# Optimization experiments

Hardware: AMD Instinct MI355X
Metric: run time of the kernel (lower is better)

Reference implementation:

```python
import jax, jax.numpy as jnp
import numpy as np

B = 32768   # batch
D = 1024    # input_dimension
H = 2048    # hidden width (layer_sizes = [2048, 2048])
LN_EPS = 1e-5


def _layer_norm(h, g, b):
    m = jnp.mean(h, axis=-1, keepdims=True)
    v = jnp.var(h, axis=-1, keepdims=True)
    return (h - m) * jax.lax.rsqrt(v + LN_EPS) * g + b


def setup_inputs() -> dict:
    key = jax.random.key(0)
    ks = jax.random.split(key, 5)
    s1 = 1.0 / np.sqrt(D)
    s2 = 1.0 / np.sqrt(H)
    return {
        "x": jax.random.normal(ks[0], (B, D), dtype=jnp.float32),
        "W1": jax.random.uniform(ks[1], (D, H), jnp.float32, -s1, s1),
        "b1": jax.random.uniform(ks[2], (H,), jnp.float32, -s1, s1),
        "g1": jnp.ones((H,), jnp.float32),
        "be1": jnp.zeros((H,), jnp.float32),
        "W2": jax.random.uniform(ks[3], (H, 9), jnp.float32, -s2, s2),
        "b2": jax.random.uniform(ks[4], (9,), jnp.float32, -s2, s2),
        "g2": jnp.ones((9,), jnp.float32),
        "be2": jnp.zeros((9,), jnp.float32),
    }


def reference(x, W1, b1, g1, be1, W2, b2, g2, be2):
    # MLP: Linear -> ReLU -> LayerNorm, twice (final width 9)
    h = _layer_norm(jax.nn.relu(x @ W1 + b1), g1, be1)      # [B, H]
    r = _layer_norm(jax.nn.relu(h @ W2 + b2), g2, be2)      # [B, 9]
    R = r.reshape(x.shape[0], 3, 3)                          # [B, 3, 3]
    # SVD projection onto SO(3): U @ diag(1,1,det(U Vh)) @ Vh
    U, _, Vh = jnp.linalg.svd(R, full_matrices=False)
    d = jnp.linalg.det(U @ Vh)                               # [B]
    scale = jnp.stack([jnp.ones_like(d), jnp.ones_like(d), d], axis=-1)  # [B,3]
    return (U * scale[:, None, :]) @ Vh                      # scale last col of U
```

## Files before the change

### kernel.cpp

```cpp
#include <hip/hip_runtime.h>

typedef unsigned short u16;
typedef _Float16 f16x8 __attribute__((ext_vector_type(8)));
typedef float f32x4 __attribute__((ext_vector_type(4)));

#define GLD16(gptr, lptr)                                                              \
  __builtin_amdgcn_global_load_lds((const __attribute__((address_space(1))) void*)(gptr), \
                                   (__attribute__((address_space(3))) void*)(lptr), 16, 0, 0)

#define MFMA_F16(a, b, c) __builtin_amdgcn_mfma_f32_16x16x32_f16((a), (b), (c), 0, 0, 0)

__global__ __launch_bounds__(256) void k_split_w1t(const float* __restrict__ w1,
                                                   u16* __restrict__ wh, u16* __restrict__ wl) {
  __shared__ float tile[32][33];
  int bn = blockIdx.x & 63;
  int bk = blockIdx.x >> 6;
  int tn = threadIdx.x & 31, tq = threadIdx.x >> 5;
#pragma unroll
  for (int r = 0; r < 4; ++r) {
    int k = bk * 32 + tq + r * 8;
    tile[tq + r * 8][tn] = w1[(size_t)k * 2048 + bn * 32 + tn];
  }
  __syncthreads();
#pragma unroll
  for (int r = 0; r < 4; ++r) {
    int n = bn * 32 + tq + r * 8;
    float v = tile[tn][tq + r * 8];
    _Float16 hi = (_Float16)v;
    _Float16 lo = (_Float16)(v - (float)hi);
    int qp = (tn >> 3) ^ ((n >> 1) & 3);
    int kp = bk * 32 + qp * 8 + (tn & 7);
    wh[(size_t)n * 1024 + kp] = __builtin_bit_cast(u16, hi);
    wl[(size_t)n * 1024 + kp] = __builtin_bit_cast(u16, lo);
  }
}

__global__ __launch_bounds__(256) void k_w2frag(const float* __restrict__ w2, const float* __restrict__ g1,
                                                u16* __restrict__ fh, u16* __restrict__ fl) {
  int t = blockIdx.x * 256 + threadIdx.x;
  int c = t >> 6, l = t & 63;
  int col = l & 15, lg = l >> 4;
  f16x8 H, L;
#pragma unroll
  for (int j = 0; j < 8; ++j) {
    int k = c * 32 + lg * 8 + j;
    float v = (col < 9) ? g1[k] * w2[k * 9 + col] : 0.f;
    _Float16 hi = (_Float16)v;
    H[j] = hi;
    L[j] = (_Float16)(v - (float)hi);
  }
  *(f16x8*)(fh + (size_t)t * 8) = H;
  *(f16x8*)(fl + (size_t)t * 8) = L;
}

__global__ void k_cgcb(const float* __restrict__ w2, const float* __restrict__ g1,
                       const float* __restrict__ be1, double* __restrict__ cgcb) {
  int l = threadIdx.x;
  double cg[9], cb[9];
#pragma unroll
  for (int j = 0; j < 9; ++j) { cg[j] = 0.0; cb[j] = 0.0; }
  for (int i = 0; i < 32; ++i) {
    int k = i * 64 + l;
    double g = (double)g1[k], b = (double)be1[k];
#pragma unroll
    for (int j = 0; j < 9; ++j) {
      double w = (double)w2[k * 9 + j];
      cg[j] += g * w;
      cb[j] += b * w;
    }
  }
  for (int off = 32; off; off >>= 1) {
#pragma unroll
    for (int j = 0; j < 9; ++j) {
      cg[j] += __shfl_xor(cg[j], off, 64);
      cb[j] += __shfl_xor(cb[j], off, 64);
    }
  }
  if (l == 0) {
    for (int j = 0; j < 16; ++j) {
      cgcb[j] = (j < 9) ? cg[j] : 0.0;
      cgcb[16 + j] = (j < 9) ? cb[j] : 0.0;
    }
  }
}

__global__ __launch_bounds__(512, 2) void k_gemm1(const float* __restrict__ x,
                                                  const u16* __restrict__ wh, const u16* __restrict__ wl,
                                                  const float* __restrict__ b1,
                                                  const u16* __restrict__ fh, const u16* __restrict__ fl,
                                                  float* __restrict__ pdot, float* __restrict__ pstat) {
  __shared__ __align__(16) u16 lds[2][32768];
  const int tid = threadIdx.x;
  const int swz = ((blockIdx.x & 7) << 7) | (blockIdx.x >> 3);
  const int m0 = (swz >> 3) << 8;
  const int n0 = (swz & 7) << 8;
  const int lane = tid & 63, w = tid >> 6;
  const int wr = (w >> 2) << 7;
  const int wc = (w & 3) << 6;
  const int lr = lane & 15, lg = lane >> 4;

  int a_off0[8], a_off1[8];
#pragma unroll
  for (int i = 0; i < 8; ++i) {
    int row = wr + i * 16 + lr;
    a_off0[i] = row * 32 + (((2 * lg) ^ (row & 7)) << 2);
    a_off1[i] = row * 32 + (((2 * lg + 1) ^ (row & 7)) << 2);
  }
  int b_off[4];
#pragma unroll
  for (int j = 0; j < 4; ++j) {
    int row = wc + j * 16 + lr;
    b_off[j] = row * 32 + ((lg ^ ((row >> 1) & 3)) << 3);
  }

  const size_t sA = (size_t)(m0 + (tid >> 3)) * 1024 + ((((tid & 7) ^ ((tid >> 3) & 7))) << 2);
  const size_t boff = (size_t)(n0 + (tid >> 2)) * 1024 + ((tid & 3) << 3);

#define STAGE_A(bf, kk)                                       \
  do {                                                        \
    GLD16(x + sA + (kk),          &lds[bf][tid * 8]);         \
    GLD16(x + sA + 65536 + (kk),  &lds[bf][4096 + tid * 8]);  \
    GLD16(x + sA + 131072 + (kk), &lds[bf][8192 + tid * 8]);  \
    GLD16(x + sA + 196608 + (kk), &lds[bf][12288 + tid * 8]); \
  } while (0)
#define STAGE_B(bf, rb, src, kk)                                       \
  do {                                                                 \
    GLD16((src) + boff + (kk),          &lds[bf][(rb) + tid * 8]);     \
    GLD16((src) + boff + 131072 + (kk), &lds[bf][(rb) + 4096 + tid * 8]); \
  } while (0)

  STAGE_A(0, 0);
  STAGE_B(0, 16384, wh, 0);
  STAGE_B(0, 24576, wl, 0);

  f32x4 acc[8][4] = {};
#pragma unroll 2
  for (int kt = 0; kt < 32; ++kt) {
    const int cur = kt & 1, nxt = cur ^ 1;
    const int nk = (kt < 31 ? kt + 1 : 31) * 32;
    STAGE_A(nxt, nk);
    asm volatile("s_waitcnt vmcnt(4)" ::: "memory");
    __builtin_amdgcn_s_barrier();
    asm volatile("" ::: "memory");
    const float* Ax = (const float*)&lds[cur][0];
    const u16* Bh = &lds[cur][16384];
    const u16* Bl = &lds[cur][24576];
    f16x8 bhf[4], blf[4], ahf[4], alf[4];

#define RD_B(j)                                         \
  do {                                                  \
    bhf[j] = *(const f16x8*)(Bh + b_off[j]);            \
    blf[j] = *(const f16x8*)(Bl + b_off[j]);            \
  } while (0)
#define RD_A(s, i)                                                    \
  do {                                                                \
    float4 fa = *(const float4*)(Ax + a_off0[i]);                     \
    float4 fb = *(const float4*)(Ax + a_off1[i]);                     \
    float ff[8] = {fa.x, fa.y, fa.z, fa.w, fb.x, fb.y, fb.z, fb.w};   \
    _Pragma("unroll")                                                 \
    for (int e = 0; e < 8; ++e) {                                     \
      _Float16 hi = (_Float16)ff[e];                                  \
      ahf[s][e] = hi;                                                 \
      alf[s][e] = (_Float16)(ff[e] - (float)hi);                      \
    }                                                                 \
  } while (0)
#define MM(s, i, j)                                     \
  do {                                                  \
    acc[i][j] = MFMA_F16(ahf[s], bhf[j], acc[i][j]);    \
    acc[i][j] = MFMA_F16(ahf[s], blf[j], acc[i][j]);    \
    acc[i][j] = MFMA_F16(alf[s], bhf[j], acc[i][j]);    \
  } while (0)
#define PRIO1 __builtin_amdgcn_s_setprio(1)
#define PRIO0 __builtin_amdgcn_s_setprio(0)

    RD_B(0); RD_A(0, 0);
    PRIO1; MM(0, 0, 0); PRIO0;
    RD_A(1, 1);
    PRIO1; MM(1, 1, 0); PRIO0;
    RD_B(1);
    STAGE_B(nxt, 16384, wh, nk);
    PRIO1; MM(0, 0, 1); MM(1, 1, 1); PRIO0;
    RD_A(2, 2);
    PRIO1; MM(2, 2, 0); MM(2, 2, 1); PRIO0;
    RD_A(3, 3);
    PRIO1; MM(3, 3, 0); MM(3, 3, 1); PRIO0;
    RD_B(2);
    STAGE_B(nxt, 24576, wl, nk);
    PRIO1; MM(0, 0, 2); MM(1, 1, 2); MM(2, 2, 2); MM(3, 3, 2); PRIO0;
    RD_B(3);
    PRIO1; MM(0, 0, 3); MM(1, 1, 3); MM(2, 2, 3); MM(3, 3, 3); PRIO0;
    RD_A(0, 4);
    PRIO1; MM(0, 4, 0); MM(0, 4, 1); MM(0, 4, 2); MM(0, 4, 3); PRIO0;
    RD_A(1, 5);
    PRIO1; MM(1, 5, 0); MM(1, 5, 1); MM(1, 5, 2); MM(1, 5, 3); PRIO0;
    RD_A(2, 6);
    PRIO1; MM(2, 6, 0); MM(2, 6, 1); MM(2, 6, 2); MM(2, 6, 3); PRIO0;
    RD_A(3, 7);
    PRIO1; MM(3, 7, 0); MM(3, 7, 1); MM(3, 7, 2); MM(3, 7, 3); PRIO0;
#undef RD_B
#undef RD_A
#undef MM
#undef PRIO1
#undef PRIO0
    asm volatile("" ::: "memory");
    __builtin_amdgcn_s_barrier();
  }
#undef STAGE_A
#undef STAGE_B

  asm volatile("s_waitcnt vmcnt(0)" ::: "memory");
  __syncthreads();
  float* vt = (float*)&lds[0][0];

#pragma unroll
  for (int j = 0; j < 4; ++j) {
    const float bias = b1[n0 + wc + j * 16 + lr];
#pragma unroll
    for (int i = 0; i < 8; ++i)
#pragma unroll
      for (int r = 0; r < 4; ++r) acc[i][j][r] = fmaxf(acc[i][j][r] + bias, 0.f);
  }

  f32x4 acc2[2] = {};
  float sstat[2] = {0.f, 0.f}, qstat[2] = {0.f, 0.f};
  const int myrow0 = w * 32;

#pragma unroll
  for (int half = 0; half < 2; ++half) {
    if (((w & 3) >> 1) == half) {
      const int colbase = wc & 127;
#pragma unroll
      for (int j = 0; j < 4; ++j) {
        const int lcol = colbase + j * 16 + lr;
        const int g = lcol >> 2, wsel = lcol & 3;
#pragma unroll
        for (int i = 0; i < 8; ++i)
#pragma unroll
          for (int r = 0; r < 4; ++r) {
            const int row = wr + i * 16 + lg * 4 + r;
            vt[row * 128 + ((g ^ (row & 7)) << 2) + wsel] = acc[i][j][r];
          }
      }
    }
    __syncthreads();
#pragma unroll
    for (int cl = 0; cl < 4; ++cl) {
      const int cglob = (n0 >> 5) + half * 4 + cl;
      const f16x8 bh = *(const f16x8*)(fh + (size_t)(cglob * 64 + lane) * 8);
      const f16x8 bl = *(const f16x8*)(fl + (size_t)(cglob * 64 + lane) * 8);
#pragma unroll
      for (int g2 = 0; g2 < 2; ++g2) {
        const int row = myrow0 + g2 * 16 + lr;
        const int g0 = cl * 8 + lg * 2;
        const float4 f0 = *(const float4*)&vt[row * 128 + ((g0 ^ (row & 7)) << 2)];
        const float4 f1 = *(const float4*)&vt[row * 128 + (((g0 + 1) ^ (row & 7)) << 2)];
        float f[8] = {f0.x, f0.y, f0.z, f0.w, f1.x, f1.y, f1.z, f1.w};
        f16x8 AH, AL;
#pragma unroll
        for (int e = 0; e < 8; ++e) {
          sstat[g2] += f[e];
          qstat[g2] = fmaf(f[e], f[e], qstat[g2]);
          _Float16 hi = (_Float16)f[e];
          AH[e] = hi;
          AL[e] = (_Float16)(f[e] - (float)hi);
        }
        acc2[g2] = MFMA_F16(AH, bh, acc2[g2]);
        acc2[g2] = MFMA_F16(AH, bl, acc2[g2]);
        acc2[g2] = MFMA_F16(AL, bh, acc2[g2]);
      }
    }
    __syncthreads();
  }

#pragma unroll
  for (int g2 = 0; g2 < 2; ++g2) {
    sstat[g2] += __shfl_xor(sstat[g2], 16, 64);
    sstat[g2] += __shfl_xor(sstat[g2], 32, 64);
    qstat[g2] += __shfl_xor(qstat[g2], 16, 64);
    qstat[g2] += __shfl_xor(qstat[g2], 32, 64);
  }
  const int ntile = n0 >> 8;
#pragma unroll
  for (int g2 = 0; g2 < 2; ++g2) {
    if (lg == 0) {
      const int row = m0 + myrow0 + g2 * 16 + lr;
      *(float2*)&pstat[((size_t)row * 8 + ntile) * 2] = make_float2(sstat[g2], qstat[g2]);
    }
    if (lr < 9) {
#pragma unroll
      for (int r = 0; r < 4; ++r) {
        const int row = m0 + myrow0 + g2 * 16 + lg * 4 + r;
        pdot[((size_t)row * 8 + ntile) * 12 + lr] = acc2[g2][r];
      }
    }
  }
}

static __device__ __forceinline__ void jrot(double S[3][3], double V[3][3], int p, int q, int r) {
  double apq = S[p][q];
  if (apq == 0.0) return;
  double tau = (S[q][q] - S[p][p]) / (2.0 * apq);
  double t = (tau >= 0.0 ? 1.0 : -1.0) / (fabs(tau) + sqrt(1.0 + tau * tau));
  double c = 1.0 / sqrt(1.0 + t * t);
  double s = t * c;
  double spp = S[p][p], sqq = S[q][q];
  double srp = S[r][p], srq = S[r][q];
  S[p][p] = spp - t * apq;
  S[q][q] = sqq + t * apq;
  S[p][q] = 0.0; S[q][p] = 0.0;
  S[r][p] = c * srp - s * srq; S[p][r] = S[r][p];
  S[r][q] = s * srp + c * srq; S[q][r] = S[r][q];
#pragma unroll
  for (int i = 0; i < 3; ++i) {
    double vip = V[i][p], viq = V[i][q];
    V[i][p] = c * vip - s * viq;
    V[i][q] = s * vip + c * viq;
  }
}

static __device__ void svd_so3(const double* Rf, float* Of) {
  double A[3][3], S[3][3];
  double V[3][3] = {{1, 0, 0}, {0, 1, 0}, {0, 0, 1}};
#pragma unroll
  for (int i = 0; i < 3; ++i)
#pragma unroll
    for (int j = 0; j < 3; ++j) A[i][j] = Rf[i * 3 + j];
#pragma unroll
  for (int p = 0; p < 3; ++p)
#pragma unroll
    for (int q = 0; q < 3; ++q) {
      double sa = 0.0;
#pragma unroll
      for (int i = 0; i < 3; ++i) sa += A[i][p] * A[i][q];
      S[p][q] = sa;
    }
  for (int it = 0; it < 6; ++it) {
    jrot(S, V, 0, 1, 2);
    jrot(S, V, 0, 2, 1);
    jrot(S, V, 1, 2, 0);
  }
  double l0 = S[0][0], l1 = S[1][1], l2 = S[2][2];
  double c0[3] = {V[0][0], V[1][0], V[2][0]};
  double c1[3] = {V[0][1], V[1][1], V[2][1]};
  double c2[3] = {V[0][2], V[1][2], V[2][2]};
  double tl, tv;
#define SWP(la, lb, ca, cb)                                         \
  if (la < lb) {                                                    \
    tl = la; la = lb; lb = tl;                                      \
    tv = ca[0]; ca[0] = cb[0]; cb[0] = tv;                          \
    tv = ca[1]; ca[1] = cb[1]; cb[1] = tv;                          \
    tv = ca[2]; ca[2] = cb[2]; cb[2] = tv;                          \
  }
  SWP(l0, l1, c0, c1)
  SWP(l0, l2, c0, c2)
  SWP(l1, l2, c1, c2)
#undef SWP
  double v3[3];
  v3[0] = c0[1] * c1[2] - c0[2] * c1[1];
  v3[1] = c0[2] * c1[0] - c0[0] * c1[2];
  v3[2] = c0[0] * c1[1] - c0[1] * c1[0];
  double t1[3], t2[3];
#pragma unroll
  for (int i = 0; i < 3; ++i) {
    t1[i] = A[i][0] * c0[0] + A[i][1] * c0[1] + A[i][2] * c0[2];
    t2[i] = A[i][0] * c1[0] + A[i][1] * c1[1] + A[i][2] * c1[2];
  }
  double n1 = sqrt(t1[0] * t1[0] + t1[1] * t1[1] + t1[2] * t1[2]);
  if (n1 < 1e-20) {
#pragma unroll
    for (int t = 0; t < 9; ++t) Of[t] = (t == 0 || t == 4 || t == 8) ? 1.f : 0.f;
    return;
  }
  double u1[3], u2[3], u3[3];
  double r1 = 1.0 / n1;
#pragma unroll
  for (int i = 0; i < 3; ++i) u1[i] = t1[i] * r1;
  double d12 = u1[0] * t2[0] + u1[1] * t2[1] + u1[2] * t2[2];
#pragma unroll
  for (int i = 0; i < 3; ++i) t2[i] -= d12 * u1[i];
  double n2 = sqrt(t2[0] * t2[0] + t2[1] * t2[1] + t2[2] * t2[2]);
  if (n2 > 1e-14 * n1) {
    double r2 = 1.0 / n2;
#pragma unroll
    for (int i = 0; i < 3; ++i) u2[i] = t2[i] * r2;
  } else {
    double ax = fabs(u1[0]), ay = fabs(u1[1]), az = fabs(u1[2]);
    double e[3] = {0.0, 0.0, 0.0};
    if (ax <= ay && ax <= az) e[0] = 1.0;
    else if (ay <= az) e[1] = 1.0;
    else e[2] = 1.0;
    double d = e[0] * u1[0] + e[1] * u1[1] + e[2] * u1[2];
#pragma unroll
    for (int i = 0; i < 3; ++i) e[i] -= d * u1[i];
    double nn = 1.0 / sqrt(e[0] * e[0] + e[1] * e[1] + e[2] * e[2]);
#pragma unroll
    for (int i = 0; i < 3; ++i) u2[i] = e[i] * nn;
  }
  u3[0] = u1[1] * u2[2] - u1[2] * u2[1];
  u3[1] = u1[2] * u2[0] - u1[0] * u2[2];
  u3[2] = u1[0] * u2[1] - u1[1] * u2[0];
#pragma unroll
  for (int i = 0; i < 3; ++i)
#pragma unroll
    for (int j = 0; j < 3; ++j)
      Of[i * 3 + j] = (float)(u1[i] * c0[j] + u2[i] * c1[j] + u3[i] * v3[j]);
}

__global__ __launch_bounds__(256) void k_comb(const float* __restrict__ pdot,
                                              const float* __restrict__ pstat,
                                              const double* __restrict__ cgcb,
                                              const float* __restrict__ b2,
                                              const float* __restrict__ g2v,
                                              const float* __restrict__ be2,
                                              float* __restrict__ out) {
  const int row = blockIdx.x * 256 + threadIdx.x;
  double dj[9];
#pragma unroll
  for (int j = 0; j < 9; ++j) dj[j] = 0.0;
  double s = 0.0, q = 0.0;
#pragma unroll
  for (int nt = 0; nt < 8; ++nt) {
    const float* p = pdot + ((size_t)row * 8 + nt) * 12;
#pragma unroll
    for (int j = 0; j < 9; ++j) dj[j] += (double)p[j];
    const float* ps = pstat + ((size_t)row * 8 + nt) * 2;
    s += (double)ps[0];
    q += (double)ps[1];
  }
  const double mean = s * (1.0 / 2048.0);
  const double varr = fmax(q * (1.0 / 2048.0) - mean * mean, 0.0);
  const double inv = 1.0 / sqrt(varr + 1e-5);
  double a2[9];
  double s9 = 0.0, q9 = 0.0;
#pragma unroll
  for (int j = 0; j < 9; ++j) {
    double v = inv * (dj[j] - mean * cgcb[j]) + cgcb[16 + j] + (double)b2[j];
    v = fmax(v, 0.0);
    a2[j] = v;
    s9 += v;
    q9 += v * v;
  }
  const double m2 = s9 * (1.0 / 9.0);
  const double v2c = fmax(q9 * (1.0 / 9.0) - m2 * m2, 0.0);
  const double i2 = 1.0 / sqrt(v2c + 1e-5);
  double rn[9];
#pragma unroll
  for (int j = 0; j < 9; ++j) rn[j] = (a2[j] - m2) * i2 * (double)g2v[j] + (double)be2[j];
  float O[9];
  svd_so3(rn, O);
  float* op = out + (size_t)row * 9;
#pragma unroll
  for (int t = 0; t < 9; ++t) op[t] = O[t];
}

extern "C" void kernel_launch(void* const* d_in, const int* in_sizes, int n_in,
                              void* d_out, int out_size, void* d_ws, size_t ws_size,
                              hipStream_t stream) {
  const float* x   = (const float*)d_in[0];
  const float* W1  = (const float*)d_in[1];
  const float* b1  = (const float*)d_in[2];
  const float* g1  = (const float*)d_in[3];
  const float* be1 = (const float*)d_in[4];
  const float* W2  = (const float*)d_in[5];
  const float* b2  = (const float*)d_in[6];
  const float* g2  = (const float*)d_in[7];
  const float* be2 = (const float*)d_in[8];
  float* out = (float*)d_out;
  char* ws = (char*)d_ws;
  u16*    wh   = (u16*)(ws + 134217728);
  u16*    wl   = (u16*)(ws + 138412032);
  u16*    fh   = (u16*)(ws + 142606336);
  u16*    fl   = (u16*)(ws + 142671872);
  double* cgcb = (double*)(ws + 142737408);
  float*  pdot = (float*)(ws + 142737664);
  float*  pstat= (float*)(ws + 155320576);

  k_split_w1t<<<dim3(2048), dim3(256), 0, stream>>>(W1, wh, wl);
  k_w2frag<<<dim3(16), dim3(256), 0, stream>>>(W2, g1, fh, fl);
  k_cgcb<<<dim3(1), dim3(64), 0, stream>>>(W2, g1, be1, cgcb);
  k_gemm1<<<dim3(1024), dim3(512), 0, stream>>>(x, wh, wl, b1, fh, fl, pdot, pstat);
  k_comb<<<dim3(128), dim3(256), 0, stream>>>(pdot, pstat, cgcb, b2, g2, be2, out);
}
```

Before: 430.0 us.

## Split x to fp16 hi/lo once at staging via register prefetch, not per wave

Changes the A-operand path in the first GEMM. x tiles are now loaded into registers two k-steps ahead, converted to fp16 hi/lo pairs once, and stored into LDS as f16. Before, fp32 tiles were loaded straight into LDS and every wave redid the conversion when reading its fragments. This removes redundant conversion ALU work and halves the LDS bytes read for A, at the cost of more VGPRs for the prefetch registers and a register-staged store path. Workspace offsets are also compacted.

```diff
diff --git a/kernel.cpp b/kernel.cpp
--- a/kernel.cpp
+++ b/kernel.cpp
@@ -89,7 +89,7 @@
                                                   const float* __restrict__ b1,
                                                   const u16* __restrict__ fh, const u16* __restrict__ fl,
                                                   float* __restrict__ pdot, float* __restrict__ pstat) {
-  __shared__ __align__(16) u16 lds[2][32768];
+  __shared__ __align__(16) u16 lds[2][4][8192];
   const int tid = threadIdx.x;
   const int swz = ((blockIdx.x & 7) << 7) | (blockIdx.x >> 3);
   const int m0 = (swz >> 3) << 8;
@@ -99,118 +99,144 @@
   const int wc = (w & 3) << 6;
   const int lr = lane & 15, lg = lane >> 4;
 
-  int a_off0[8], a_off1[8];
+  int a_off[8], b_off[4];
 #pragma unroll
   for (int i = 0; i < 8; ++i) {
     int row = wr + i * 16 + lr;
-    a_off0[i] = row * 32 + (((2 * lg) ^ (row & 7)) << 2);
-    a_off1[i] = row * 32 + (((2 * lg + 1) ^ (row & 7)) << 2);
-  }
-  int b_off[4];
+    a_off[i] = row * 32 + ((lg ^ ((row >> 1) & 3)) << 3);
+  }
 #pragma unroll
   for (int j = 0; j < 4; ++j) {
     int row = wc + j * 16 + lr;
     b_off[j] = row * 32 + ((lg ^ ((row >> 1) & 3)) << 3);
   }
 
-  const size_t sA = (size_t)(m0 + (tid >> 3)) * 1024 + ((((tid & 7) ^ ((tid >> 3) & 7))) << 2);
+  const size_t sxa_lo = (size_t)(m0 + (tid >> 2)) * 1024 + (size_t)(((tid & 3) ^ ((tid >> 3) & 3)) << 3);
+  const size_t sxa_hi = sxa_lo + (size_t)128 * 1024;
   const size_t boff = (size_t)(n0 + (tid >> 2)) * 1024 + ((tid & 3) << 3);
 
-#define STAGE_A(bf, kk)                                       \
-  do {                                                        \
-    GLD16(x + sA + (kk),          &lds[bf][tid * 8]);         \
-    GLD16(x + sA + 65536 + (kk),  &lds[bf][4096 + tid * 8]);  \
-    GLD16(x + sA + 131072 + (kk), &lds[bf][8192 + tid * 8]);  \
-    GLD16(x + sA + 196608 + (kk), &lds[bf][12288 + tid * 8]); \
-  } while (0)
-#define STAGE_B(bf, rb, src, kk)                                       \
-  do {                                                                 \
-    GLD16((src) + boff + (kk),          &lds[bf][(rb) + tid * 8]);     \
-    GLD16((src) + boff + 131072 + (kk), &lds[bf][(rb) + 4096 + tid * 8]); \
-  } while (0)
-
-  STAGE_A(0, 0);
-  STAGE_B(0, 16384, wh, 0);
-  STAGE_B(0, 24576, wl, 0);
+#define STAGE_B(bf, mt, src, kk)                                          \
+  do {                                                                    \
+    GLD16((src) + boff + (kk), &lds[bf][mt][tid * 8]);                    \
+    GLD16((src) + boff + 131072 + (kk), &lds[bf][mt][4096 + tid * 8]);    \
+  } while (0)
+
+#define LOAD_A(REG, kk)                                                   \
+  do {                                                                    \
+    REG[0] = *(const float4*)(x + sxa_lo + (kk));                         \
+    REG[1] = *(const float4*)(x + sxa_lo + (kk) + 4);                     \
+    REG[2] = *(const float4*)(x + sxa_hi + (kk));                         \
+    REG[3] = *(const float4*)(x + sxa_hi + (kk) + 4);                     \
+  } while (0)
+
+#define CVT_STORE(bf, REG)                                                \
+  do {                                                                    \
+    float ff0[8] = {REG[0].x, REG[0].y, REG[0].z, REG[0].w,               \
+                    REG[1].x, REG[1].y, REG[1].z, REG[1].w};              \
+    float ff1[8] = {REG[2].x, REG[2].y, REG[2].z, REG[2].w,               \
+                    REG[3].x, REG[3].y, REG[3].z, REG[3].w};              \
+    f16x8 H0, L0, H1, L1;                                                 \
+    _Pragma("unroll")                                                     \
+    for (int e = 0; e < 8; ++e) {                                         \
+      _Float16 h0 = (_Float16)ff0[e];                                     \
+      H0[e] = h0;                                                         \
+      L0[e] = (_Float16)(ff0[e] - (float)h0);                             \
+      _Float16 h1 = (_Float16)ff1[e];                                     \
+      H1[e] = h1;                                                         \
+      L1[e] = (_Float16)(ff1[e] - (float)h1);                             \
+    }                                                                     \
+    *(f16x8*)&lds[bf][0][tid * 8] = H0;                                   \
+    *(f16x8*)&lds[bf][1][tid * 8] = L0;                                   \
+    *(f16x8*)&lds[bf][0][4096 + tid * 8] = H1;                            \
+    *(f16x8*)&lds[bf][1][4096 + tid * 8] = L1;                            \
+  } while (0)
+
+  float4 regA[4], regB[4];
+
+  LOAD_A(regA, 0);
+  LOAD_A(regB, 32);
+  STAGE_B(0, 2, wh, 0);
+  STAGE_B(0, 3, wl, 0);
+  asm volatile("s_waitcnt vmcnt(8)" ::: "memory");
+  CVT_STORE(0, regA);
 
   f32x4 acc[8][4] = {};
-#pragma unroll 2
-  for (int kt = 0; kt < 32; ++kt) {
-    const int cur = kt & 1, nxt = cur ^ 1;
-    const int nk = (kt < 31 ? kt + 1 : 31) * 32;
-    STAGE_A(nxt, nk);
-    asm volatile("s_waitcnt vmcnt(4)" ::: "memory");
-    __builtin_amdgcn_s_barrier();
-    asm volatile("" ::: "memory");
-    const float* Ax = (const float*)&lds[cur][0];
-    const u16* Bh = &lds[cur][16384];
-    const u16* Bl = &lds[cur][24576];
-    f16x8 bhf[4], blf[4], ahf[4], alf[4];
-
-#define RD_B(j)                                         \
-  do {                                                  \
-    bhf[j] = *(const f16x8*)(Bh + b_off[j]);            \
-    blf[j] = *(const f16x8*)(Bl + b_off[j]);            \
-  } while (0)
-#define RD_A(s, i)                                                    \
-  do {                                                                \
-    float4 fa = *(const float4*)(Ax + a_off0[i]);                     \
-    float4 fb = *(const float4*)(Ax + a_off1[i]);                     \
-    float ff[8] = {fa.x, fa.y, fa.z, fa.w, fb.x, fb.y, fb.z, fb.w};   \
-    _Pragma("unroll")                                                 \
-    for (int e = 0; e < 8; ++e) {                                     \
-      _Float16 hi = (_Float16)ff[e];                                  \
-      ahf[s][e] = hi;                                                 \
-      alf[s][e] = (_Float16)(ff[e] - (float)hi);                      \
-    }                                                                 \
-  } while (0)
-#define MM(s, i, j)                                     \
-  do {                                                  \
-    acc[i][j] = MFMA_F16(ahf[s], bhf[j], acc[i][j]);    \
-    acc[i][j] = MFMA_F16(ahf[s], blf[j], acc[i][j]);    \
-    acc[i][j] = MFMA_F16(alf[s], bhf[j], acc[i][j]);    \
+
+#define RD_B(CUR, j)                                      \
+  do {                                                    \
+    bhf[j] = *(const f16x8*)(&lds[CUR][2][0] + b_off[j]); \
+    blf[j] = *(const f16x8*)(&lds[CUR][3][0] + b_off[j]); \
+  } while (0)
+#define RD_A(CUR, s, i)                                   \
+  do {                                                    \
+    ahf[s] = *(const f16x8*)(&lds[CUR][0][0] + a_off[i]); \
+    alf[s] = *(const f16x8*)(&lds[CUR][1][0] + a_off[i]); \
+  } while (0)
+#define MM(s, i, j)                                       \
+  do {                                                    \
+    acc[i][j] = MFMA_F16(ahf[s], bhf[j], acc[i][j]);      \
+    acc[i][j] = MFMA_F16(ahf[s], blf[j], acc[i][j]);      \
+    acc[i][j] = MFMA_F16(alf[s], bhf[j], acc[i][j]);      \
   } while (0)
 #define PRIO1 __builtin_amdgcn_s_setprio(1)
 #define PRIO0 __builtin_amdgcn_s_setprio(0)
 
-    RD_B(0); RD_A(0, 0);
-    PRIO1; MM(0, 0, 0); PRIO0;
-    RD_A(1, 1);
-    PRIO1; MM(1, 1, 0); PRIO0;
-    RD_B(1);
-    STAGE_B(nxt, 16384, wh, nk);
-    PRIO1; MM(0, 0, 1); MM(1, 1, 1); PRIO0;
-    RD_A(2, 2);
-    PRIO1; MM(2, 2, 0); MM(2, 2, 1); PRIO0;
-    RD_A(3, 3);
-    PRIO1; MM(3, 3, 0); MM(3, 3, 1); PRIO0;
-    RD_B(2);
-    STAGE_B(nxt, 24576, wl, nk);
-    PRIO1; MM(0, 0, 2); MM(1, 1, 2); MM(2, 2, 2); MM(3, 3, 2); PRIO0;
-    RD_B(3);
-    PRIO1; MM(0, 0, 3); MM(1, 1, 3); MM(2, 2, 3); MM(3, 3, 3); PRIO0;
-    RD_A(0, 4);
-    PRIO1; MM(0, 4, 0); MM(0, 4, 1); MM(0, 4, 2); MM(0, 4, 3); PRIO0;
-    RD_A(1, 5);
-    PRIO1; MM(1, 5, 0); MM(1, 5, 1); MM(1, 5, 2); MM(1, 5, 3); PRIO0;
-    RD_A(2, 6);
-    PRIO1; MM(2, 6, 0); MM(2, 6, 1); MM(2, 6, 2); MM(2, 6, 3); PRIO0;
-    RD_A(3, 7);
-    PRIO1; MM(3, 7, 0); MM(3, 7, 1); MM(3, 7, 2); MM(3, 7, 3); PRIO0;
+#define KBODY(KT, CUR, NXT, RLOAD, RCVT)                                            \
+  do {                                                                              \
+    const int nk1 = ((KT) + 1 < 32 ? (KT) + 1 : 31) * 32;                           \
+    const int nk2 = ((KT) + 2 < 32 ? (KT) + 2 : 31) * 32;                           \
+    LOAD_A(RLOAD, nk2);                                        \
+    asm volatile("s_waitcnt vmcnt(8)" ::: "memory");        \
+    CVT_STORE(NXT, RCVT);                                  \
+    asm volatile("s_waitcnt vmcnt(4)" ::: "memory");              \
+    __builtin_amdgcn_s_barrier();                         \
+    asm volatile("" ::: "memory");                                                  \
+    f16x8 bhf[4], blf[4], ahf[4], alf[4];                                           \
+    RD_B(CUR, 0); RD_A(CUR, 0, 0);                                                  \
+    PRIO1; MM(0, 0, 0); PRIO0;                                                      \
+    RD_A(CUR, 1, 1);                                                                \
+    PRIO1; MM(1, 1, 0); PRIO0;                                                      \
+    RD_B(CUR, 1);                                                                   \
+    PRIO1; MM(0, 0, 1); MM(1, 1, 1); PRIO0;                                         \
+    RD_A(CUR, 2, 2);                                                                \
+    PRIO1; MM(2, 2, 0); MM(2, 2, 1); PRIO0;                                         \
+    RD_A(CUR, 3, 3);                                                                \
+    PRIO1; MM(3, 3, 0); MM(3, 3, 1); PRIO0;                                         \
+    RD_B(CUR, 2);                                                                   \
+    STAGE_B(NXT, 2, wh, nk1);                                                       \
+    PRIO1; MM(0, 0, 2); MM(1, 1, 2); MM(2, 2, 2); MM(3, 3, 2); PRIO0;               \
+    RD_B(CUR, 3);                                                                   \
+    STAGE_B(NXT, 3, wl, nk1);                                                       \
+    PRIO1; MM(0, 0, 3); MM(1, 1, 3); MM(2, 2, 3); MM(3, 3, 3); PRIO0;               \
+    RD_A(CUR, 0, 4);                                                                \
+    PRIO1; MM(0, 4, 0); MM(0, 4, 1); MM(0, 4, 2); MM(0, 4, 3); PRIO0;               \
+    RD_A(CUR, 1, 5);                                                                \
+    PRIO1; MM(1, 5, 0); MM(1, 5, 1); MM(1, 5, 2); MM(1, 5, 3); PRIO0;               \
+    RD_A(CUR, 2, 6);                                                                \
+    PRIO1; MM(2, 6, 0); MM(2, 6, 1); MM(2, 6, 2); MM(2, 6, 3); PRIO0;               \
+    RD_A(CUR, 3, 7);                                                                \
+    PRIO1; MM(3, 7, 0); MM(3, 7, 1); MM(3, 7, 2); MM(3, 7, 3); PRIO0;               \
+    asm volatile("" ::: "memory");                                                  \
+    __builtin_amdgcn_s_barrier();              \
+  } while (0)
+
+  for (int kt2 = 0; kt2 < 16; ++kt2) {
+    KBODY(2 * kt2,     0, 1, regA, regB);
+    KBODY(2 * kt2 + 1, 1, 0, regB, regA);
+  }
+#undef KBODY
 #undef RD_B
 #undef RD_A
 #undef MM
 #undef PRIO1
 #undef PRIO0
-    asm volatile("" ::: "memory");
-    __builtin_amdgcn_s_barrier();
-  }
-#undef STAGE_A
 #undef STAGE_B
+#undef LOAD_A
+#undef CVT_STORE
 
   asm volatile("s_waitcnt vmcnt(0)" ::: "memory");
   __syncthreads();
-  float* vt = (float*)&lds[0][0];
+  float* vt = (float*)&lds[0][0][0];
 
 #pragma unroll
   for (int j = 0; j < 4; ++j) {
@@ -467,13 +493,13 @@
   const float* be2 = (const float*)d_in[8];
   float* out = (float*)d_out;
   char* ws = (char*)d_ws;
-  u16*    wh   = (u16*)(ws + 134217728);
-  u16*    wl   = (u16*)(ws + 138412032);
-  u16*    fh   = (u16*)(ws + 142606336);
-  u16*    fl   = (u16*)(ws + 142671872);
-  double* cgcb = (double*)(ws + 142737408);
-  float*  pdot = (float*)(ws + 142737664);
-  float*  pstat= (float*)(ws + 155320576);
+  u16*    wh   = (u16*)(ws + 0);
+  u16*    wl   = (u16*)(ws + 4194304);
+  u16*    fh   = (u16*)(ws + 8388608);
+  u16*    fl   = (u16*)(ws + 8454144);
+  double* cgcb = (double*)(ws + 8519680);
+  float*  pdot = (float*)(ws + 8519936);
+  float*  pstat= (float*)(ws + 21102848);
 
   k_split_w1t<<<dim3(2048), dim3(256), 0, stream>>>(W1, wh, wl);
   k_w2frag<<<dim3(16), dim3(256), 0, stream>>>(W2, g1, fh, fl);
```

New measurement: 392.8 us. -8.6%, faster.
